# Kernel optimization log

Hardware: AMD Instinct MI355X
Metric: run time of the kernel (lower is better)

The kernel has to match this reference:

```python
import jax, jax.numpy as jnp
import numpy as np
import math

D_MODEL = 768
N_HEAD = 12
D_FF = 3072
LN_EPS = 1e-5


def gelu_new(x):
    return 0.5 * x * (1.0 + jnp.tanh(jnp.sqrt(2.0 / jnp.pi) * (x + 0.044715 * x ** 3)))


def layer_norm(x, g, b):
    mu = jnp.mean(x, axis=-1, keepdims=True)
    var = jnp.mean(jnp.square(x - mu), axis=-1, keepdims=True)
    return (x - mu) * jax.lax.rsqrt(var + LN_EPS) * g + b


def setup_inputs() -> dict:
    key = jax.random.key(0)
    ks = jax.random.split(key, 8)
    B, S = 4, 2048
    x = jax.random.normal(ks[0], (B, S, D_MODEL), dtype=jnp.float32)
    # causal look-ahead mask: 1 = attend, 0 = masked
    look_ahead_mask = jnp.tril(jnp.ones((S, S), dtype=jnp.float32))[None, None]
    std = 0.02
    Wqkv = jax.random.normal(ks[1], (D_MODEL, 3 * D_MODEL), dtype=jnp.float32) * std
    bqkv = jnp.zeros((3 * D_MODEL,), dtype=jnp.float32)
    Wo = jax.random.normal(ks[2], (D_MODEL, D_MODEL), dtype=jnp.float32) * std
    bo = jnp.zeros((D_MODEL,), dtype=jnp.float32)
    Wfc = jax.random.normal(ks[3], (D_MODEL, D_FF), dtype=jnp.float32) * std
    bfc = jnp.zeros((D_FF,), dtype=jnp.float32)
    Wpr = jax.random.normal(ks[4], (D_FF, D_MODEL), dtype=jnp.float32) * std
    bpr = jnp.zeros((D_MODEL,), dtype=jnp.float32)
    g1 = jnp.ones((D_MODEL,), dtype=jnp.float32)
    b1 = jnp.zeros((D_MODEL,), dtype=jnp.float32)
    g2 = jnp.ones((D_MODEL,), dtype=jnp.float32)
    b2 = jnp.zeros((D_MODEL,), dtype=jnp.float32)
    return dict(x=x, look_ahead_mask=look_ahead_mask, Wqkv=Wqkv, bqkv=bqkv,
                Wo=Wo, bo=bo, Wfc=Wfc, bfc=bfc, Wpr=Wpr, bpr=bpr,
                g1=g1, b1=b1, g2=g2, b2=b2)


def reference(x, look_ahead_mask, Wqkv, bqkv, Wo, bo, Wfc, bfc, Wpr, bpr, g1, b1, g2, b2):
    B, S, D = x.shape
    dk = D // N_HEAD
    # --- attention sublayer (dropout = identity, eval mode) ---
    nx = layer_norm(x, g1, b1)
    qkv = nx @ Wqkv + bqkv                       # [B,S,3D]
    q, k, v = jnp.split(qkv, 3, axis=-1)
    def heads(t):
        return t.reshape(B, S, N_HEAD, dk).transpose(0, 2, 1, 3)  # [B,H,S,dk]
    q, k, v = heads(q), heads(k), heads(v)
    scores = jnp.einsum('bhqd,bhkd->bhqk', q, k) / jnp.sqrt(jnp.float32(dk))
    scores = scores + (1.0 - look_ahead_mask) * -10000.0
    attn_scores = jax.nn.softmax(scores, axis=-1)  # [B,H,S,S]
    out = jnp.einsum('bhqk,bhkd->bhqd', attn_scores, v)
    out = out.transpose(0, 2, 1, 3).reshape(B, S, D)
    a = out @ Wo + bo
    x = x + a
    # --- MLP sublayer ---
    h = layer_norm(x, g2, b2)
    m = gelu_new(h @ Wfc + bfc) @ Wpr + bpr
    x = x + m
    return (x, attn_scores)
```

## Files before the change

kernel.cpp:

```cpp
#include <hip/hip_runtime.h>
#include <stdint.h>

#define D_MODEL 768
#define NHEAD   12
#define DKH     64
#define SEQ     2048
#define BATCH   4
#define DFF     3072
#define NROWS   (BATCH*SEQ)

typedef __bf16 bf16x8 __attribute__((ext_vector_type(8)));
typedef float  f32x4  __attribute__((ext_vector_type(4)));

__device__ __forceinline__ unsigned short f2bf(float f) {
  union { float f; unsigned int u; } v; v.f = f;
  unsigned int r = v.u + 0x7fffu + ((v.u >> 16) & 1u);
  return (unsigned short)(r >> 16);
}

__device__ __forceinline__ void gl_lds16(const void* g, void* l) {
  __builtin_amdgcn_global_load_lds(
      (__attribute__((address_space(1))) void*)(uintptr_t)g,
      (__attribute__((address_space(3))) void*)(uintptr_t)l, 16, 0, 0);
}

__global__ __launch_bounds__(256) void k_wtrans(const float* __restrict__ W,
                                               unsigned short* __restrict__ Wt,
                                               int K, int N) {
  __shared__ float tile[32][33];
  int n0 = blockIdx.x * 32, k0 = blockIdx.y * 32;
  int c = threadIdx.x & 31, r = threadIdx.x >> 5;
#pragma unroll
  for (int i = 0; i < 4; ++i)
    tile[r + i * 8][c] = W[(size_t)(k0 + r + i * 8) * N + n0 + c];
  __syncthreads();
#pragma unroll
  for (int i = 0; i < 4; ++i)
    Wt[(size_t)(n0 + r + i * 8) * K + k0 + c] = f2bf(tile[c][r + i * 8]);
}

__global__ __launch_bounds__(256) void k_ln(const float* __restrict__ x,
                                            const float* __restrict__ g,
                                            const float* __restrict__ bb,
                                            unsigned short* __restrict__ y) {
  int row = blockIdx.x, t = threadIdx.x;
  const float* xr = x + (size_t)row * D_MODEL;
  float v0 = xr[t], v1 = xr[t + 256], v2 = xr[t + 512];
  float s = v0 + v1 + v2;
  float s2 = v0 * v0 + v1 * v1 + v2 * v2;
#pragma unroll
  for (int off = 32; off >= 1; off >>= 1) {
    s  += __shfl_xor(s, off, 64);
    s2 += __shfl_xor(s2, off, 64);
  }
  __shared__ float rs_[4], rs2_[4];
  int w = t >> 6;
  if ((t & 63) == 0) { rs_[w] = s; rs2_[w] = s2; }
  __syncthreads();
  s  = rs_[0] + rs_[1] + rs_[2] + rs_[3];
  s2 = rs2_[0] + rs2_[1] + rs2_[2] + rs2_[3];
  float mu  = s * (1.0f / D_MODEL);
  float var = s2 * (1.0f / D_MODEL) - mu * mu;
  float rstd = rsqrtf(var + 1e-5f);
  unsigned short* yr = y + (size_t)row * D_MODEL;
  yr[t]       = f2bf((v0 - mu) * rstd * g[t]       + bb[t]);
  yr[t + 256] = f2bf((v1 - mu) * rstd * g[t + 256] + bb[t + 256]);
  yr[t + 512] = f2bf((v2 - mu) * rstd * g[t + 512] + bb[t + 512]);
}

#define EPI_QKV 0
#define EPI_WO  1
#define EPI_FC  2
#define EPI_PR  3

template <int EPI>
__global__ __launch_bounds__(256) void k_gemm(
    const unsigned short* __restrict__ A,
    const unsigned short* __restrict__ Bt,
    const float* __restrict__ bias,
    const float* __restrict__ res,
    float* __restrict__ outf,
    unsigned short* __restrict__ outb,
    unsigned short* __restrict__ qo,
    unsigned short* __restrict__ ko,
    unsigned short* __restrict__ vto,
    int K, int N) {
  __shared__ __align__(16) unsigned char smem[36864];
  unsigned short* As = (unsigned short*)smem;
  unsigned short* Bs = (unsigned short*)(smem + 16384);
  int t = threadIdx.x;
  int l = t & 63, w = t >> 6;
  int wm = w >> 1, wn = w & 1;
  int m0 = blockIdx.y * 128, n0 = blockIdx.x * 128;
  int lr = l & 15, lg = l >> 4;

  const f32x4 fz = {0.0f, 0.0f, 0.0f, 0.0f};
  f32x4 acc[4][4];
#pragma unroll
  for (int i = 0; i < 4; ++i)
#pragma unroll
    for (int j = 0; j < 4; ++j) acc[i][j] = fz;

  int arow = t >> 3;
  int aslot = t & 7;
  const unsigned short* Ag = A + (size_t)(m0 + arow) * K + aslot * 8;
  const unsigned short* Bg = Bt + (size_t)(n0 + arow) * K + aslot * 8;
  int ntile = K >> 6;

  for (int kt = 0; kt < ntile; ++kt) {
    const unsigned short* Agk = Ag + kt * 64;
    const unsigned short* Bgk = Bg + kt * 64;
#pragma unroll
    for (int i = 0; i < 4; ++i)
      gl_lds16(Agk + (size_t)i * 32 * K, As + (i * 256 + t) * 8);
#pragma unroll
    for (int i = 0; i < 4; ++i)
      gl_lds16(Bgk + (size_t)i * 32 * K, Bs + (i * 256 + t) * 8);
    __syncthreads();
#pragma unroll
    for (int ks = 0; ks < 2; ++ks) {
      bf16x8 af[4], bf_[4];
#pragma unroll
      for (int i = 0; i < 4; ++i)
        af[i] = *(const bf16x8*)(As + (wm * 64 + i * 16 + lr) * 64 + ks * 32 + lg * 8);
#pragma unroll
      for (int i = 0; i < 4; ++i)
        bf_[i] = *(const bf16x8*)(Bs + (wn * 64 + i * 16 + lr) * 64 + ks * 32 + lg * 8);
#pragma unroll
      for (int i = 0; i < 4; ++i)
#pragma unroll
        for (int j = 0; j < 4; ++j)
          acc[i][j] = __builtin_amdgcn_mfma_f32_16x16x32_bf16(af[i], bf_[j], acc[i][j], 0, 0, 0);
    }
    __syncthreads();
  }

  int mb = m0 + wm * 64;
  int nb = n0 + wn * 64;

  if constexpr (EPI == EPI_WO || EPI == EPI_PR) {
#pragma unroll
    for (int i = 0; i < 4; ++i)
#pragma unroll
      for (int r = 0; r < 4; ++r) {
        int m = mb + i * 16 + 4 * lg + r;
#pragma unroll
        for (int j = 0; j < 4; ++j) {
          int n = nb + j * 16 + lr;
          outf[(size_t)m * D_MODEL + n] = acc[i][j][r] + bias[n] + res[(size_t)m * D_MODEL + n];
        }
      }
  } else if constexpr (EPI == EPI_FC) {
#pragma unroll
    for (int i = 0; i < 4; ++i)
#pragma unroll
      for (int r = 0; r < 4; ++r) {
        int m = mb + i * 16 + 4 * lg + r;
#pragma unroll
        for (int j = 0; j < 4; ++j) {
          int n = nb + j * 16 + lr;
          float u = acc[i][j][r] + bias[n];
          float c = 0.7978845608028654f * (u + 0.044715f * u * u * u);
          float gl = 0.5f * u * (1.0f + tanhf(c));
          outb[(size_t)m * DFF + n] = f2bf(gl);
        }
      }
  } else {
    int region = n0 / 768;
    int b = m0 >> 11;
    if (region < 2) {
      unsigned short* dst = (region == 0) ? qo : ko;
#pragma unroll
      for (int i = 0; i < 4; ++i)
#pragma unroll
        for (int r = 0; r < 4; ++r) {
          int m = mb + i * 16 + 4 * lg + r;
          int s = m & (SEQ - 1);
#pragma unroll
          for (int j = 0; j < 4; ++j) {
            int n = nb + j * 16 + lr;
            int nl = n - region * 768;
            int h = nl >> 6, d = nl & 63;
            dst[(((size_t)(b * NHEAD + h) * SEQ + s) << 6) + d] = f2bf(acc[i][j][r] + bias[n]);
          }
        }
    } else {
      int nl = nb - 1536;
      int h = nl >> 6;
      unsigned short* Tw = (unsigned short*)(smem + w * 9216);
#pragma unroll
      for (int j = 0; j < 4; ++j) {
        int dcol = j * 16 + lr;
        int n = nb + j * 16 + lr;
#pragma unroll
        for (int i = 0; i < 4; ++i)
#pragma unroll
          for (int r = 0; r < 4; ++r)
            Tw[dcol * 72 + i * 16 + 4 * lg + r] = f2bf(acc[i][j][r] + bias[n]);
      }
      __syncthreads();
      int srow = l >> 3, sc = (l & 7) * 8;
      int s0 = mb & (SEQ - 1);
#pragma unroll
      for (int i = 0; i < 8; ++i) {
        int d = i * 8 + srow;
        bf16x8 vv = *(const bf16x8*)(Tw + d * 72 + sc);
        *(bf16x8*)(vto + ((size_t)(b * NHEAD + h) * DKH + d) * SEQ + s0 + sc) = vv;
      }
    }
  }
}

template <int WRITEP>
__global__ __launch_bounds__(256) void k_attn(const unsigned short* __restrict__ q,
                                              const unsigned short* __restrict__ kk,
                                              const unsigned short* __restrict__ vt,
                                              float* __restrict__ lsumbuf,
                                              float* __restrict__ attn,
                                              unsigned short* __restrict__ ao) {
  __shared__ __align__(16) unsigned short Ks[64 * 64];
  __shared__ __align__(16) unsigned short Vts[64 * 64];
  __shared__ __align__(16) unsigned short Pw[4][16 * 72];
  int t = threadIdx.x, l = t & 63, w = t >> 6;
  int lr = l & 15, lg = l >> 4;
  int qt = blockIdx.x, bh = blockIdx.y;
  int q0 = qt * 64;
  int qrow0 = q0 + w * 16;

  const unsigned short* qbase = q + ((size_t)bh * SEQ + qrow0 + lr) * DKH;
  bf16x8 aq0 = *(const bf16x8*)(qbase + lg * 8);
  bf16x8 aq1 = *(const bf16x8*)(qbase + 32 + lg * 8);

  const f32x4 fz = {0.0f, 0.0f, 0.0f, 0.0f};
  float lsum[4] = {0.f, 0.f, 0.f, 0.f};

  for (int kt = 0; kt <= qt; ++kt) {
#pragma unroll
    for (int i = 0; i < 2; ++i) {
      int lin = i * 256 + t;
      gl_lds16(kk + ((size_t)bh * SEQ + kt * 64 + (lin >> 3)) * DKH + (lin & 7) * 8,
               Ks + lin * 8);
    }
    __syncthreads();
    f32x4 sacc[4];
#pragma unroll
    for (int f = 0; f < 4; ++f) sacc[f] = fz;
#pragma unroll
    for (int f = 0; f < 4; ++f) {
      bf16x8 bk0 = *(const bf16x8*)(Ks + (f * 16 + lr) * 64 + lg * 8);
      sacc[f] = __builtin_amdgcn_mfma_f32_16x16x32_bf16(aq0, bk0, sacc[f], 0, 0, 0);
      bf16x8 bk1 = *(const bf16x8*)(Ks + (f * 16 + lr) * 64 + 32 + lg * 8);
      sacc[f] = __builtin_amdgcn_mfma_f32_16x16x32_bf16(aq1, bk1, sacc[f], 0, 0, 0);
    }
#pragma unroll
    for (int r = 0; r < 4; ++r) {
      int qg = qrow0 + 4 * lg + r;
      float rsum = 0.f;
#pragma unroll
      for (int f = 0; f < 4; ++f) {
        int ksg = kt * 64 + f * 16 + lr;
        float s = sacc[f][r] * 0.125f;
        if (ksg > qg) s -= 10000.0f;
        rsum += expf(s);
      }
      rsum += __shfl_xor(rsum, 1, 64);
      rsum += __shfl_xor(rsum, 2, 64);
      rsum += __shfl_xor(rsum, 4, 64);
      rsum += __shfl_xor(rsum, 8, 64);
      lsum[r] += rsum;
    }
    __syncthreads();
  }
  float invl[4];
#pragma unroll
  for (int r = 0; r < 4; ++r) {
    invl[r] = 1.0f / lsum[r];
    if (WRITEP == 0 && lr == 0)
      lsumbuf[(size_t)bh * SEQ + qrow0 + 4 * lg + r] = lsum[r];
  }

  f32x4 oacc[4];
#pragma unroll
  for (int f = 0; f < 4; ++f) oacc[f] = fz;

  unsigned short* Pme = Pw[w];
  for (int kt = 0; kt <= qt; ++kt) {
#pragma unroll
    for (int i = 0; i < 2; ++i) {
      int lin = i * 256 + t;
      gl_lds16(kk + ((size_t)bh * SEQ + kt * 64 + (lin >> 3)) * DKH + (lin & 7) * 8,
               Ks + lin * 8);
      gl_lds16(vt + ((size_t)bh * DKH + (lin >> 3)) * SEQ + kt * 64 + (lin & 7) * 8,
               Vts + lin * 8);
    }
    __syncthreads();
    f32x4 sacc[4];
#pragma unroll
    for (int f = 0; f < 4; ++f) sacc[f] = fz;
#pragma unroll
    for (int f = 0; f < 4; ++f) {
      bf16x8 bk0 = *(const bf16x8*)(Ks + (f * 16 + lr) * 64 + lg * 8);
      sacc[f] = __builtin_amdgcn_mfma_f32_16x16x32_bf16(aq0, bk0, sacc[f], 0, 0, 0);
      bf16x8 bk1 = *(const bf16x8*)(Ks + (f * 16 + lr) * 64 + 32 + lg * 8);
      sacc[f] = __builtin_amdgcn_mfma_f32_16x16x32_bf16(aq1, bk1, sacc[f], 0, 0, 0);
    }
#pragma unroll
    for (int r = 0; r < 4; ++r) {
      int qg = qrow0 + 4 * lg + r;
#pragma unroll
      for (int f = 0; f < 4; ++f) {
        int ksg = kt * 64 + f * 16 + lr;
        float s = sacc[f][r] * 0.125f;
        if (ksg > qg) s -= 10000.0f;
        float p = expf(s) * invl[r];
        if (WRITEP) attn[((size_t)bh * SEQ + qg) * SEQ + ksg] = p;
        Pme[(4 * lg + r) * 72 + f * 16 + lr] = f2bf(p);
      }
    }
    __syncthreads();
#pragma unroll
    for (int ds = 0; ds < 2; ++ds) {
      bf16x8 ap = *(const bf16x8*)(Pme + lr * 72 + ds * 32 + lg * 8);
#pragma unroll
      for (int f = 0; f < 4; ++f) {
        bf16x8 bv = *(const bf16x8*)(Vts + (f * 16 + lr) * 64 + ds * 32 + lg * 8);
        oacc[f] = __builtin_amdgcn_mfma_f32_16x16x32_bf16(ap, bv, oacc[f], 0, 0, 0);
      }
    }
    __syncthreads();
  }

  if (WRITEP) {
    int zstart = (qt + 1) * 64;
#pragma unroll
    for (int r = 0; r < 4; ++r) {
      int qg = qrow0 + 4 * lg + r;
      float* rowp = attn + ((size_t)bh * SEQ + qg) * SEQ;
      for (int c = zstart + lr * 4; c < SEQ; c += 64)
        *(float4*)(rowp + c) = make_float4(0.f, 0.f, 0.f, 0.f);
    }
  }

  int b = bh / NHEAD, h = bh % NHEAD;
#pragma unroll
  for (int r = 0; r < 4; ++r) {
    int qg = qrow0 + 4 * lg + r;
#pragma unroll
    for (int f = 0; f < 4; ++f)
      ao[(size_t)(b * SEQ + qg) * D_MODEL + h * DKH + f * 16 + lr] = f2bf(oacc[f][r]);
  }
}

__global__ __launch_bounds__(256) void k_pwrite(const unsigned short* __restrict__ q,
                                                const unsigned short* __restrict__ kk,
                                                const float* __restrict__ lsumbuf,
                                                float* __restrict__ attn) {
  __shared__ __align__(16) unsigned short Ks[64 * 64];
  int t = threadIdx.x, l = t & 63, w = t >> 6;
  int lr = l & 15, lg = l >> 4;
  int qt = blockIdx.x, bh = blockIdx.y;
  int qrow0 = qt * 64 + w * 16;

  const unsigned short* qbase = q + ((size_t)bh * SEQ + qrow0 + lr) * DKH;
  bf16x8 aq0 = *(const bf16x8*)(qbase + lg * 8);
  bf16x8 aq1 = *(const bf16x8*)(qbase + 32 + lg * 8);

  float invl[4];
#pragma unroll
  for (int r = 0; r < 4; ++r)
    invl[r] = 1.0f / lsumbuf[(size_t)bh * SEQ + qrow0 + 4 * lg + r];

  const f32x4 fz = {0.0f, 0.0f, 0.0f, 0.0f};
  for (int kt = 0; kt <= qt; ++kt) {
#pragma unroll
    for (int i = 0; i < 2; ++i) {
      int lin = i * 256 + t;
      gl_lds16(kk + ((size_t)bh * SEQ + kt * 64 + (lin >> 3)) * DKH + (lin & 7) * 8,
               Ks + lin * 8);
    }
    __syncthreads();
    f32x4 sacc[4];
#pragma unroll
    for (int f = 0; f < 4; ++f) sacc[f] = fz;
#pragma unroll
    for (int f = 0; f < 4; ++f) {
      bf16x8 bk0 = *(const bf16x8*)(Ks + (f * 16 + lr) * 64 + lg * 8);
      sacc[f] = __builtin_amdgcn_mfma_f32_16x16x32_bf16(aq0, bk0, sacc[f], 0, 0, 0);
      bf16x8 bk1 = *(const bf16x8*)(Ks + (f * 16 + lr) * 64 + 32 + lg * 8);
      sacc[f] = __builtin_amdgcn_mfma_f32_16x16x32_bf16(aq1, bk1, sacc[f], 0, 0, 0);
    }
#pragma unroll
    for (int r = 0; r < 4; ++r) {
      int qg = qrow0 + 4 * lg + r;
#pragma unroll
      for (int f = 0; f < 4; ++f) {
        int ksg = kt * 64 + f * 16 + lr;
        float s = sacc[f][r] * 0.125f;
        if (ksg > qg) s -= 10000.0f;
        attn[((size_t)bh * SEQ + qg) * SEQ + ksg] = expf(s) * invl[r];
      }
    }
    __syncthreads();
  }

  int zstart = (qt + 1) * 64;
#pragma unroll
  for (int r = 0; r < 4; ++r) {
    int qg = qrow0 + 4 * lg + r;
    float* rowp = attn + ((size_t)bh * SEQ + qg) * SEQ;
    for (int c = zstart + lr * 4; c < SEQ; c += 64)
      *(float4*)(rowp + c) = make_float4(0.f, 0.f, 0.f, 0.f);
  }
}

extern "C" void kernel_launch(void* const* d_in, const int* in_sizes, int n_in,
                              void* d_out, int out_size, void* d_ws, size_t ws_size,
                              hipStream_t stream) {
  (void)in_sizes; (void)n_in; (void)out_size;
  const float* x    = (const float*)d_in[0];
  const float* Wqkv = (const float*)d_in[2];
  const float* bqkv = (const float*)d_in[3];
  const float* Wo   = (const float*)d_in[4];
  const float* bo   = (const float*)d_in[5];
  const float* Wfc  = (const float*)d_in[6];
  const float* bfc  = (const float*)d_in[7];
  const float* Wpr  = (const float*)d_in[8];
  const float* bpr  = (const float*)d_in[9];
  const float* g1   = (const float*)d_in[10];
  const float* b1   = (const float*)d_in[11];
  const float* g2   = (const float*)d_in[12];
  const float* b2   = (const float*)d_in[13];

  float* outx = (float*)d_out;
  float* attn = outx + (size_t)NROWS * D_MODEL;

  char* ws = (char*)d_ws;
  dim3 blk(256);

  const size_t NEED_FUSED = 77070336;
  if (ws_size >= NEED_FUSED + 65536) {
    unsigned short* qb    = (unsigned short*)(ws + 0);
    unsigned short* kb    = (unsigned short*)(ws + 12582912);
    unsigned short* vtb   = (unsigned short*)(ws + 25165824);
    unsigned short* m1    = (unsigned short*)(ws + 0);
    unsigned short* nx    = (unsigned short*)(ws + 50331648);
    unsigned short* ao    = (unsigned short*)(ws + 50331648);
    unsigned short* hb    = (unsigned short*)(ws + 50331648);
    unsigned short* WqkvT = (unsigned short*)(ws + 62914560);
    unsigned short* WoT   = (unsigned short*)(ws + 66453504);
    unsigned short* WfcT  = (unsigned short*)(ws + 67633152);
    unsigned short* WprT  = (unsigned short*)(ws + 72351744);
    float*          x1    = outx;

    k_wtrans<<<dim3(2304 / 32, 768 / 32), blk, 0, stream>>>(Wqkv, WqkvT, 768, 2304);
    k_wtrans<<<dim3(768 / 32, 768 / 32), blk, 0, stream>>>(Wo, WoT, 768, 768);
    k_wtrans<<<dim3(3072 / 32, 768 / 32), blk, 0, stream>>>(Wfc, WfcT, 768, 3072);
    k_wtrans<<<dim3(768 / 32, 3072 / 32), blk, 0, stream>>>(Wpr, WprT, 3072, 768);

    k_ln<<<NROWS, blk, 0, stream>>>(x, g1, b1, nx);

    k_gemm<EPI_QKV><<<dim3(2304 / 128, NROWS / 128), blk, 0, stream>>>(
        nx, WqkvT, bqkv, nullptr, nullptr, nullptr, qb, kb, vtb, 768, 2304);

    k_attn<1><<<dim3(SEQ / 64, BATCH * NHEAD), blk, 0, stream>>>(
        qb, kb, vtb, nullptr, attn, ao);

    k_gemm<EPI_WO><<<dim3(768 / 128, NROWS / 128), blk, 0, stream>>>(
        ao, WoT, bo, x, x1, nullptr, nullptr, nullptr, nullptr, 768, 768);

    k_ln<<<NROWS, blk, 0, stream>>>(x1, g2, b2, hb);

    k_gemm<EPI_FC><<<dim3(3072 / 128, NROWS / 128), blk, 0, stream>>>(
        hb, WfcT, bfc, nullptr, nullptr, m1, nullptr, nullptr, nullptr, 768, 3072);

    k_gemm<EPI_PR><<<dim3(768 / 128, NROWS / 128), blk, 0, stream>>>(
        m1, WprT, bpr, x1, outx, nullptr, nullptr, nullptr, nullptr, 3072, 768);
  } else {
    size_t off = 0;
    auto alloc = [&](size_t bytes) {
      char* p = ws + off;
      off += (bytes + 255) & ~(size_t)255;
      return p;
    };
    unsigned short* qb   = (unsigned short*)alloc((size_t)NROWS * D_MODEL * 2);
    unsigned short* kb   = (unsigned short*)alloc((size_t)NROWS * D_MODEL * 2);
    float*          lsum = (float*)alloc((size_t)BATCH * NHEAD * SEQ * 4);

    char* aws = (char*)attn;
    size_t aoff = 0;
    auto aalloc = [&](size_t bytes) {
      char* p = aws + aoff;
      aoff += (bytes + 255) & ~(size_t)255;
      return p;
    };
    unsigned short* WqkvT = (unsigned short*)aalloc((size_t)2304 * 768 * 2);
    unsigned short* WoT   = (unsigned short*)aalloc((size_t)768 * 768 * 2);
    unsigned short* WfcT  = (unsigned short*)aalloc((size_t)3072 * 768 * 2);
    unsigned short* WprT  = (unsigned short*)aalloc((size_t)768 * 3072 * 2);
    unsigned short* nx    = (unsigned short*)aalloc((size_t)NROWS * D_MODEL * 2);
    unsigned short* vtb   = (unsigned short*)aalloc((size_t)NROWS * D_MODEL * 2);
    unsigned short* ao    = (unsigned short*)aalloc((size_t)NROWS * D_MODEL * 2);
    float*          x1    = (float*)aalloc((size_t)NROWS * D_MODEL * 4);
    unsigned short* hb    = (unsigned short*)aalloc((size_t)NROWS * D_MODEL * 2);
    unsigned short* m1    = (unsigned short*)aalloc((size_t)NROWS * DFF * 2);

    k_wtrans<<<dim3(2304 / 32, 768 / 32), blk, 0, stream>>>(Wqkv, WqkvT, 768, 2304);
    k_wtrans<<<dim3(768 / 32, 768 / 32), blk, 0, stream>>>(Wo, WoT, 768, 768);
    k_wtrans<<<dim3(3072 / 32, 768 / 32), blk, 0, stream>>>(Wfc, WfcT, 768, 3072);
    k_wtrans<<<dim3(768 / 32, 3072 / 32), blk, 0, stream>>>(Wpr, WprT, 3072, 768);

    k_ln<<<NROWS, blk, 0, stream>>>(x, g1, b1, nx);

    k_gemm<EPI_QKV><<<dim3(2304 / 128, NROWS / 128), blk, 0, stream>>>(
        nx, WqkvT, bqkv, nullptr, nullptr, nullptr, qb, kb, vtb, 768, 2304);

    k_attn<0><<<dim3(SEQ / 64, BATCH * NHEAD), blk, 0, stream>>>(
        qb, kb, vtb, lsum, nullptr, ao);

    k_gemm<EPI_WO><<<dim3(768 / 128, NROWS / 128), blk, 0, stream>>>(
        ao, WoT, bo, x, x1, nullptr, nullptr, nullptr, nullptr, 768, 768);

    k_ln<<<NROWS, blk, 0, stream>>>(x1, g2, b2, hb);

    k_gemm<EPI_FC><<<dim3(3072 / 128, NROWS / 128), blk, 0, stream>>>(
        hb, WfcT, bfc, nullptr, nullptr, m1, nullptr, nullptr, nullptr, 768, 3072);

    k_gemm<EPI_PR><<<dim3(768 / 128, NROWS / 128), blk, 0, stream>>>(
        m1, WprT, bpr, x1, outx, nullptr, nullptr, nullptr, nullptr, 3072, 768);

    k_pwrite<<<dim3(SEQ / 64, BATCH * NHEAD), blk, 0, stream>>>(qb, kb, lsum, attn);
  }
}
```

Baseline: 642.2 us.

## Enlarge attention query tile, reverse block order, fuse weight transposes, fast exp/tanh

The attention kernel now has each block handle 128 query rows (32 per wave) instead of 64, so every K/V tile loaded into LDS is reused by twice as many queries. Blocks are launched in reverse order so the longest causal rows start first. Masked scores are set to zero directly instead of calling exp on a -10000 offset, and expf becomes __expf. The four weight-transpose launches become one kernel, and GELU's tanhf is replaced by an exp-based formula. In exchange the kernel uses more registers and LDS, launches half as many attention blocks, and its exp is slightly less accurate.

```diff
diff --git a/kernel.cpp b/kernel.cpp
--- a/kernel.cpp
+++ b/kernel.cpp
@@ -24,11 +24,21 @@
       (__attribute__((address_space(3))) void*)(uintptr_t)l, 16, 0, 0);
 }
 
-__global__ __launch_bounds__(256) void k_wtrans(const float* __restrict__ W,
-                                               unsigned short* __restrict__ Wt,
-                                               int K, int N) {
+__global__ __launch_bounds__(256) void k_wtrans_all(
+    const float* __restrict__ Wqkv, const float* __restrict__ Wo,
+    const float* __restrict__ Wfc, const float* __restrict__ Wpr,
+    unsigned short* __restrict__ WqkvT, unsigned short* __restrict__ WoT,
+    unsigned short* __restrict__ WfcT, unsigned short* __restrict__ WprT) {
+  int id = blockIdx.x;
+  const float* W; unsigned short* Wt; int K, N, tid;
+  if (id < 1728)      { W = Wqkv; Wt = WqkvT; K = 768;  N = 2304; tid = id; }
+  else if (id < 2304) { W = Wo;   Wt = WoT;   K = 768;  N = 768;  tid = id - 1728; }
+  else if (id < 4608) { W = Wfc;  Wt = WfcT;  K = 768;  N = 3072; tid = id - 2304; }
+  else                { W = Wpr;  Wt = WprT;  K = 3072; N = 768;  tid = id - 4608; }
+  int ntn = N / 32;
+  int n0 = (tid % ntn) * 32, k0 = (tid / ntn) * 32;
+
   __shared__ float tile[32][33];
-  int n0 = blockIdx.x * 32, k0 = blockIdx.y * 32;
   int c = threadIdx.x & 31, r = threadIdx.x >> 5;
 #pragma unroll
   for (int i = 0; i < 4; ++i)
@@ -161,7 +171,11 @@
           int n = nb + j * 16 + lr;
           float u = acc[i][j][r] + bias[n];
           float c = 0.7978845608028654f * (u + 0.044715f * u * u * u);
-          float gl = 0.5f * u * (1.0f + tanhf(c));
+          float a2 = fabsf(c);
+          float e = __expf(-2.0f * a2);
+          float th = (1.0f - e) / (1.0f + e);
+          th = (c < 0.0f) ? -th : th;
+          float gl = 0.5f * u * (1.0f + th);
           outb[(size_t)m * DFF + n] = f2bf(gl);
         }
       }
@@ -220,21 +234,27 @@
                                               unsigned short* __restrict__ ao) {
   __shared__ __align__(16) unsigned short Ks[64 * 64];
   __shared__ __align__(16) unsigned short Vts[64 * 64];
-  __shared__ __align__(16) unsigned short Pw[4][16 * 72];
+  __shared__ __align__(16) unsigned short Pw[4][32 * 72];
   int t = threadIdx.x, l = t & 63, w = t >> 6;
   int lr = l & 15, lg = l >> 4;
-  int qt = blockIdx.x, bh = blockIdx.y;
-  int q0 = qt * 64;
-  int qrow0 = q0 + w * 16;
-
-  const unsigned short* qbase = q + ((size_t)bh * SEQ + qrow0 + lr) * DKH;
-  bf16x8 aq0 = *(const bf16x8*)(qbase + lg * 8);
-  bf16x8 aq1 = *(const bf16x8*)(qbase + 32 + lg * 8);
+  int qt = gridDim.x - 1 - blockIdx.x;
+  int bh = blockIdx.y;
+  int q0 = qt * 128;
+  int qrow0 = q0 + w * 32;
+  int kmax = 2 * qt + 1;
+
+  bf16x8 aq[2][2];
+#pragma unroll
+  for (int m = 0; m < 2; ++m) {
+    const unsigned short* qbase = q + ((size_t)bh * SEQ + qrow0 + m * 16 + lr) * DKH;
+    aq[m][0] = *(const bf16x8*)(qbase + lg * 8);
+    aq[m][1] = *(const bf16x8*)(qbase + 32 + lg * 8);
+  }
 
   const f32x4 fz = {0.0f, 0.0f, 0.0f, 0.0f};
-  float lsum[4] = {0.f, 0.f, 0.f, 0.f};
-
-  for (int kt = 0; kt <= qt; ++kt) {
+  float lsum[2][4] = {{0.f, 0.f, 0.f, 0.f}, {0.f, 0.f, 0.f, 0.f}};
+
+  for (int kt = 0; kt <= kmax; ++kt) {
 #pragma unroll
     for (int i = 0; i < 2; ++i) {
       int lin = i * 256 + t;
@@ -242,49 +262,55 @@
                Ks + lin * 8);
     }
     __syncthreads();
-    f32x4 sacc[4];
-#pragma unroll
-    for (int f = 0; f < 4; ++f) sacc[f] = fz;
-#pragma unroll
-    for (int f = 0; f < 4; ++f) {
-      bf16x8 bk0 = *(const bf16x8*)(Ks + (f * 16 + lr) * 64 + lg * 8);
-      sacc[f] = __builtin_amdgcn_mfma_f32_16x16x32_bf16(aq0, bk0, sacc[f], 0, 0, 0);
-      bf16x8 bk1 = *(const bf16x8*)(Ks + (f * 16 + lr) * 64 + 32 + lg * 8);
-      sacc[f] = __builtin_amdgcn_mfma_f32_16x16x32_bf16(aq1, bk1, sacc[f], 0, 0, 0);
-    }
+#pragma unroll
+    for (int m = 0; m < 2; ++m) {
+      f32x4 sacc[4];
+#pragma unroll
+      for (int f = 0; f < 4; ++f) sacc[f] = fz;
+#pragma unroll
+      for (int f = 0; f < 4; ++f) {
+        bf16x8 bk0 = *(const bf16x8*)(Ks + (f * 16 + lr) * 64 + lg * 8);
+        sacc[f] = __builtin_amdgcn_mfma_f32_16x16x32_bf16(aq[m][0], bk0, sacc[f], 0, 0, 0);
+        bf16x8 bk1 = *(const bf16x8*)(Ks + (f * 16 + lr) * 64 + 32 + lg * 8);
+        sacc[f] = __builtin_amdgcn_mfma_f32_16x16x32_bf16(aq[m][1], bk1, sacc[f], 0, 0, 0);
+      }
+#pragma unroll
+      for (int r = 0; r < 4; ++r) {
+        int qg = qrow0 + m * 16 + 4 * lg + r;
+        float rsum = 0.f;
+#pragma unroll
+        for (int f = 0; f < 4; ++f) {
+          int ksg = kt * 64 + f * 16 + lr;
+          float p = (ksg <= qg) ? __expf(sacc[f][r] * 0.125f) : 0.0f;
+          rsum += p;
+        }
+        rsum += __shfl_xor(rsum, 1, 64);
+        rsum += __shfl_xor(rsum, 2, 64);
+        rsum += __shfl_xor(rsum, 4, 64);
+        rsum += __shfl_xor(rsum, 8, 64);
+        lsum[m][r] += rsum;
+      }
+    }
+    __syncthreads();
+  }
+  float invl[2][4];
+#pragma unroll
+  for (int m = 0; m < 2; ++m)
 #pragma unroll
     for (int r = 0; r < 4; ++r) {
-      int qg = qrow0 + 4 * lg + r;
-      float rsum = 0.f;
-#pragma unroll
-      for (int f = 0; f < 4; ++f) {
-        int ksg = kt * 64 + f * 16 + lr;
-        float s = sacc[f][r] * 0.125f;
-        if (ksg > qg) s -= 10000.0f;
-        rsum += expf(s);
-      }
-      rsum += __shfl_xor(rsum, 1, 64);
-      rsum += __shfl_xor(rsum, 2, 64);
-      rsum += __shfl_xor(rsum, 4, 64);
-      rsum += __shfl_xor(rsum, 8, 64);
-      lsum[r] += rsum;
-    }
-    __syncthreads();
-  }
-  float invl[4];
-#pragma unroll
-  for (int r = 0; r < 4; ++r) {
-    invl[r] = 1.0f / lsum[r];
-    if (WRITEP == 0 && lr == 0)
-      lsumbuf[(size_t)bh * SEQ + qrow0 + 4 * lg + r] = lsum[r];
-  }
-
-  f32x4 oacc[4];
-#pragma unroll
-  for (int f = 0; f < 4; ++f) oacc[f] = fz;
+      invl[m][r] = 1.0f / lsum[m][r];
+      if (WRITEP == 0 && lr == 0)
+        lsumbuf[(size_t)bh * SEQ + qrow0 + m * 16 + 4 * lg + r] = lsum[m][r];
+    }
+
+  f32x4 oacc[2][4];
+#pragma unroll
+  for (int m = 0; m < 2; ++m)
+#pragma unroll
+    for (int f = 0; f < 4; ++f) oacc[m][f] = fz;
 
   unsigned short* Pme = Pw[w];
-  for (int kt = 0; kt <= qt; ++kt) {
+  for (int kt = 0; kt <= kmax; ++kt) {
 #pragma unroll
     for (int i = 0; i < 2; ++i) {
       int lin = i * 256 + t;
@@ -294,61 +320,67 @@
                Vts + lin * 8);
     }
     __syncthreads();
-    f32x4 sacc[4];
-#pragma unroll
-    for (int f = 0; f < 4; ++f) sacc[f] = fz;
-#pragma unroll
-    for (int f = 0; f < 4; ++f) {
-      bf16x8 bk0 = *(const bf16x8*)(Ks + (f * 16 + lr) * 64 + lg * 8);
-      sacc[f] = __builtin_amdgcn_mfma_f32_16x16x32_bf16(aq0, bk0, sacc[f], 0, 0, 0);
-      bf16x8 bk1 = *(const bf16x8*)(Ks + (f * 16 + lr) * 64 + 32 + lg * 8);
-      sacc[f] = __builtin_amdgcn_mfma_f32_16x16x32_bf16(aq1, bk1, sacc[f], 0, 0, 0);
-    }
+#pragma unroll
+    for (int m = 0; m < 2; ++m) {
+      f32x4 sacc[4];
+#pragma unroll
+      for (int f = 0; f < 4; ++f) sacc[f] = fz;
+#pragma unroll
+      for (int f = 0; f < 4; ++f) {
+        bf16x8 bk0 = *(const bf16x8*)(Ks + (f * 16 + lr) * 64 + lg * 8);
+        sacc[f] = __builtin_amdgcn_mfma_f32_16x16x32_bf16(aq[m][0], bk0, sacc[f], 0, 0, 0);
+        bf16x8 bk1 = *(const bf16x8*)(Ks + (f * 16 + lr) * 64 + 32 + lg * 8);
+        sacc[f] = __builtin_amdgcn_mfma_f32_16x16x32_bf16(aq[m][1], bk1, sacc[f], 0, 0, 0);
+      }
+#pragma unroll
+      for (int r = 0; r < 4; ++r) {
+        int qg = qrow0 + m * 16 + 4 * lg + r;
+#pragma unroll
+        for (int f = 0; f < 4; ++f) {
+          int ksg = kt * 64 + f * 16 + lr;
+          float p = (ksg <= qg) ? __expf(sacc[f][r] * 0.125f) * invl[m][r] : 0.0f;
+          if (WRITEP) attn[((size_t)bh * SEQ + qg) * SEQ + ksg] = p;
+          Pme[(m * 16 + 4 * lg + r) * 72 + f * 16 + lr] = f2bf(p);
+        }
+      }
+    }
+#pragma unroll
+    for (int ds = 0; ds < 2; ++ds)
+#pragma unroll
+      for (int m = 0; m < 2; ++m) {
+        bf16x8 ap = *(const bf16x8*)(Pme + (m * 16 + lr) * 72 + ds * 32 + lg * 8);
+#pragma unroll
+        for (int f = 0; f < 4; ++f) {
+          bf16x8 bv = *(const bf16x8*)(Vts + (f * 16 + lr) * 64 + ds * 32 + lg * 8);
+          oacc[m][f] = __builtin_amdgcn_mfma_f32_16x16x32_bf16(ap, bv, oacc[m][f], 0, 0, 0);
+        }
+      }
+    __syncthreads();
+  }
+
+  if (WRITEP) {
+    int zstart = q0 + 128;
+#pragma unroll
+    for (int m = 0; m < 2; ++m)
+#pragma unroll
+      for (int r = 0; r < 4; ++r) {
+        int qg = qrow0 + m * 16 + 4 * lg + r;
+        float* rowp = attn + ((size_t)bh * SEQ + qg) * SEQ;
+        for (int c = zstart + lr * 4; c < SEQ; c += 64)
+          *(float4*)(rowp + c) = make_float4(0.f, 0.f, 0.f, 0.f);
+      }
+  }
+
+  int b = bh / NHEAD, h = bh % NHEAD;
+#pragma unroll
+  for (int m = 0; m < 2; ++m)
 #pragma unroll
     for (int r = 0; r < 4; ++r) {
-      int qg = qrow0 + 4 * lg + r;
-#pragma unroll
-      for (int f = 0; f < 4; ++f) {
-        int ksg = kt * 64 + f * 16 + lr;
-        float s = sacc[f][r] * 0.125f;
-        if (ksg > qg) s -= 10000.0f;
-        float p = expf(s) * invl[r];
-        if (WRITEP) attn[((size_t)bh * SEQ + qg) * SEQ + ksg] = p;
-        Pme[(4 * lg + r) * 72 + f * 16 + lr] = f2bf(p);
-      }
-    }
-    __syncthreads();
-#pragma unroll
-    for (int ds = 0; ds < 2; ++ds) {
-      bf16x8 ap = *(const bf16x8*)(Pme + lr * 72 + ds * 32 + lg * 8);
-#pragma unroll
-      for (int f = 0; f < 4; ++f) {
-        bf16x8 bv = *(const bf16x8*)(Vts + (f * 16 + lr) * 64 + ds * 32 + lg * 8);
-        oacc[f] = __builtin_amdgcn_mfma_f32_16x16x32_bf16(ap, bv, oacc[f], 0, 0, 0);
-      }
-    }
-    __syncthreads();
-  }
-
-  if (WRITEP) {
-    int zstart = (qt + 1) * 64;
-#pragma unroll
-    for (int r = 0; r < 4; ++r) {
-      int qg = qrow0 + 4 * lg + r;
-      float* rowp = attn + ((size_t)bh * SEQ + qg) * SEQ;
-      for (int c = zstart + lr * 4; c < SEQ; c += 64)
-        *(float4*)(rowp + c) = make_float4(0.f, 0.f, 0.f, 0.f);
-    }
-  }
-
-  int b = bh / NHEAD, h = bh % NHEAD;
-#pragma unroll
-  for (int r = 0; r < 4; ++r) {
-    int qg = qrow0 + 4 * lg + r;
-#pragma unroll
-    for (int f = 0; f < 4; ++f)
-      ao[(size_t)(b * SEQ + qg) * D_MODEL + h * DKH + f * 16 + lr] = f2bf(oacc[f][r]);
-  }
+      int qg = qrow0 + m * 16 + 4 * lg + r;
+#pragma unroll
+      for (int f = 0; f < 4; ++f)
+        ao[(size_t)(b * SEQ + qg) * D_MODEL + h * DKH + f * 16 + lr] = f2bf(oacc[m][f][r]);
+    }
 }
 
 __global__ __launch_bounds__(256) void k_pwrite(const unsigned short* __restrict__ q,
@@ -395,9 +427,8 @@
 #pragma unroll
       for (int f = 0; f < 4; ++f) {
         int ksg = kt * 64 + f * 16 + lr;
-        float s = sacc[f][r] * 0.125f;
-        if (ksg > qg) s -= 10000.0f;
-        attn[((size_t)bh * SEQ + qg) * SEQ + ksg] = expf(s) * invl[r];
+        float p = (ksg <= qg) ? __expf(sacc[f][r] * 0.125f) * invl[r] : 0.0f;
+        attn[((size_t)bh * SEQ + qg) * SEQ + ksg] = p;
       }
     }
     __syncthreads();
@@ -452,17 +483,14 @@
     unsigned short* WprT  = (unsigned short*)(ws + 72351744);
     float*          x1    = outx;
 
-    k_wtrans<<<dim3(2304 / 32, 768 / 32), blk, 0, stream>>>(Wqkv, WqkvT, 768, 2304);
-    k_wtrans<<<dim3(768 / 32, 768 / 32), blk, 0, stream>>>(Wo, WoT, 768, 768);
-    k_wtrans<<<dim3(3072 / 32, 768 / 32), blk, 0, stream>>>(Wfc, WfcT, 768, 3072);
-    k_wtrans<<<dim3(768 / 32, 3072 / 32), blk, 0, stream>>>(Wpr, WprT, 3072, 768);
+    k_wtrans_all<<<dim3(6912), blk, 0, stream>>>(Wqkv, Wo, Wfc, Wpr, WqkvT, WoT, WfcT, WprT);
 
     k_ln<<<NROWS, blk, 0, stream>>>(x, g1, b1, nx);
 
     k_gemm<EPI_QKV><<<dim3(2304 / 128, NROWS / 128), blk, 0, stream>>>(
         nx, WqkvT, bqkv, nullptr, nullptr, nullptr, qb, kb, vtb, 768, 2304);
 
-    k_attn<1><<<dim3(SEQ / 64, BATCH * NHEAD), blk, 0, stream>>>(
+    k_attn<1><<<dim3(SEQ / 128, BATCH * NHEAD), blk, 0, stream>>>(
         qb, kb, vtb, nullptr, attn, ao);
 
     k_gemm<EPI_WO><<<dim3(768 / 128, NROWS / 128), blk, 0, stream>>>(
@@ -504,17 +532,14 @@
     unsigned short* hb    = (unsigned short*)aalloc((size_t)NROWS * D_MODEL * 2);
     unsigned short* m1    = (unsigned short*)aalloc((size_t)NROWS * DFF * 2);
 
-    k_wtrans<<<dim3(2304 / 32, 768 / 32), blk, 0, stream>>>(Wqkv, WqkvT, 768, 2304);
-    k_wtrans<<<dim3(768 / 32, 768 / 32), blk, 0, stream>>>(Wo, WoT, 768, 768);
-    k_wtrans<<<dim3(3072 / 32, 768 / 32), blk, 0, stream>>>(Wfc, WfcT, 768, 3072);
-    k_wtrans<<<dim3(768 / 32, 3072 / 32), blk, 0, stream>>>(Wpr, WprT, 3072, 768);
+    k_wtrans_all<<<dim3(6912), blk, 0, stream>>>(Wqkv, Wo, Wfc, Wpr, WqkvT, WoT, WfcT, WprT);
 
     k_ln<<<NROWS, blk, 0, stream>>>(x, g1, b1, nx);
 
     k_gemm<EPI_QKV><<<dim3(2304 / 128, NROWS / 128), blk, 0, stream>>>(
         nx, WqkvT, bqkv, nullptr, nullptr, nullptr, qb, kb, vtb, 768, 2304);
 
-    k_attn<0><<<dim3(SEQ / 64, BATCH * NHEAD), blk, 0, stream>>>(
+    k_attn<0><<<dim3(SEQ / 128, BATCH * NHEAD), blk, 0, stream>>>(
         qb, kb, vtb, lsum, nullptr, ao);
 
     k_gemm<EPI_WO><<<dim3(768 / 128, NROWS / 128), blk, 0, stream>>>(
```

New measurement: 605.9 us. -5.6%, faster.
